# Optimization experiments

Hardware: AMD Instinct MI355X
Metric: run time of the kernel (lower is better)

The kernel has to match this reference:

```python
import jax, jax.numpy as jnp
import numpy as np

NUM_QUERIES, NUM_KEYS = 32, 64
QUERY_DIM, KEY_DIM = 512, 512
NUM_HEADS, ATTN_DIM = 8, 64
EMBED_DIM = NUM_HEADS * ATTN_DIM  # 512
OUT_DIM = 512
TEMPERATURE = float(np.sqrt(ATTN_DIM))


def setup_inputs() -> dict:
    key = jax.random.key(0)
    ks = jax.random.split(key, 6)
    b = 1.0 / TEMPERATURE
    b_p = 1.0 / float(np.sqrt(OUT_DIM))
    q = jax.random.normal(ks[0], (NUM_QUERIES, 2048, QUERY_DIM), dtype=jnp.float32)
    k = jax.random.normal(ks[1], (NUM_KEYS, 2048, KEY_DIM), dtype=jnp.float32)
    query_weight = jax.random.uniform(ks[2], (NUM_QUERIES, QUERY_DIM, EMBED_DIM), minval=-b, maxval=b, dtype=jnp.float32)
    key_weight = jax.random.uniform(ks[3], (NUM_KEYS, KEY_DIM, EMBED_DIM), minval=-b, maxval=b, dtype=jnp.float32)
    value_weight = jax.random.uniform(ks[4], (NUM_KEYS, KEY_DIM, EMBED_DIM), minval=-b, maxval=b, dtype=jnp.float32)
    proj_weight = jax.random.uniform(ks[5], (NUM_QUERIES, EMBED_DIM, OUT_DIM), minval=-b_p, maxval=b_p, dtype=jnp.float32)
    return {"q": q, "k": k, "query_weight": query_weight, "key_weight": key_weight,
            "value_weight": value_weight, "proj_weight": proj_weight}


def reference(q, k, query_weight, key_weight, value_weight, proj_weight):
    Qn, bs, _ = q.shape
    Kn = k.shape[0]
    H, D = NUM_HEADS, ATTN_DIM
    # per-slot projections: (slots, bs, embed) -> split embed into heads
    query = jnp.einsum('ibq,iqe->ibe', q, query_weight).reshape(Qn, bs, H, D)
    key_e = jnp.einsum('jbk,jke->jbe', k, key_weight).reshape(Kn, bs, H, D)
    value = jnp.einsum('jbk,jke->jbe', k, value_weight).reshape(Kn, bs, H, D)
    # logits over key slots per (batch, head, query slot)
    logits = jnp.einsum('ibhd,jbhd->bhij', query, key_e) / TEMPERATURE
    attn = jax.nn.softmax(logits, axis=-1)  # softmax over key slots
    out = jnp.einsum('bhij,jbhd->ibhd', attn, value).reshape(Qn, bs, H * D)
    out = jnp.einsum('ibe,ieo->ibo', out, proj_weight)
    return out
```

## Files before the change

### kernel.cpp

```cpp
#include <hip/hip_runtime.h>

typedef __attribute__((ext_vector_type(8))) short bf16x8;
typedef __attribute__((ext_vector_type(4))) float f32x4;
typedef __attribute__((ext_vector_type(4))) unsigned short us4;

__device__ __forceinline__ unsigned short f2bf(float f) {
    unsigned u = __builtin_bit_cast(unsigned, f);
    u += 0x7FFFu + ((u >> 16) & 1u);
    return (unsigned short)(u >> 16);
}

__device__ __forceinline__ void gl_lds16(const void* g, void* l) {
    __builtin_amdgcn_global_load_lds(
        (const __attribute__((address_space(1))) unsigned int*)g,
        (__attribute__((address_space(3))) unsigned int*)l, 16, 0, 0);
}

__global__ __launch_bounds__(256) void cast_f32_bf16(const float* __restrict__ in,
                                                     unsigned short* __restrict__ out, int n4) {
    int i = blockIdx.x * blockDim.x + threadIdx.x;
    int stride = gridDim.x * blockDim.x;
    for (; i < n4; i += stride) {
        float4 v = ((const float4*)in)[i];
        us4 o;
        o.x = f2bf(v.x); o.y = f2bf(v.y); o.z = f2bf(v.z); o.w = f2bf(v.w);
        ((us4*)out)[i] = o;
    }
}

__global__ __launch_bounds__(256) void transpose_w(const float* __restrict__ wq,
                                                   const float* __restrict__ wk,
                                                   const float* __restrict__ wv,
                                                   const float* __restrict__ wp,
                                                   unsigned short* __restrict__ Wt) {
    int sb = blockIdx.x >> 6;
    int tile = blockIdx.x & 63;
    const float* src;
    if (sb < 32)       src = wq + (size_t)sb * 262144;
    else if (sb < 96)  src = wk + (size_t)(sb - 32) * 262144;
    else if (sb < 160) src = wv + (size_t)(sb - 96) * 262144;
    else               src = wp + (size_t)(sb - 160) * 262144;
    unsigned short* dst = Wt + (size_t)sb * 262144;
    int q0 = (tile & 7) * 64, e0 = (tile >> 3) * 64;
    __shared__ float t[64][65];
    int tx = threadIdx.x & 63, ty = threadIdx.x >> 6;
    for (int i = 0; i < 16; i++) {
        int r = ty + 4 * i;
        t[r][tx] = src[(size_t)(q0 + r) * 512 + e0 + tx];
    }
    __syncthreads();
    int tx2 = threadIdx.x & 31, ty2 = threadIdx.x >> 5;
    for (int i = 0; i < 8; i++) {
        int e = ty2 + 8 * i;
        int qq = tx2 * 2;
        unsigned a = f2bf(t[qq][e]);
        unsigned bb = f2bf(t[qq + 1][e]);
        *(unsigned*)&dst[(size_t)(e0 + e) * 512 + q0 + qq] = a | (bb << 16);
    }
}

__device__ __forceinline__ void gemm256(const unsigned short* __restrict__ Ag,
                                        const unsigned short* __restrict__ Bg,
                                        unsigned short (&lds)[2][2][16384],
                                        f32x4 (&acc)[8][4]) {
    const int tid = threadIdx.x;
    const int l = tid & 63, wid = tid >> 6;
    const int wr = (wid >> 2) * 128, wc = (wid & 3) * 64;
    const int lr = l & 15, shi = l >> 4;
    const int srcs = ((l & 7) ^ ((l >> 3) & 7)) * 8;
    const int grow = l >> 3;

    bf16x8 af[4][2], bf[2][2][2];

#define STG_(which, hh, t) do {                                                     \
    const unsigned short* gp = (which) ? Bg : Ag;                                   \
    _Pragma("unroll")                                                               \
    for (int q = 0; q < 2; q++) {                                                   \
        int lrow = (hh) * 128 + wid * 16 + q * 8;                                   \
        gl_lds16(gp + (size_t)(lrow + grow) * 512 + (t) * 64 + srcs,                \
                 &lds[(t) & 1][which][lrow * 64]);                                  \
    } } while (0)

#define LDA_(cur, mh) do {                                                          \
    _Pragma("unroll") for (int m = 0; m < 4; m++)                                   \
    _Pragma("unroll") for (int ks = 0; ks < 2; ks++)                                \
        af[m][ks] = *(const bf16x8*)&lds[cur][0]                                    \
            [(wr + (mh) * 64 + m * 16 + lr) * 64 + ((ks * 4 + shi) ^ (l & 7)) * 8]; \
    } while (0)

#define LDB_(cur, nh) do {                                                          \
    _Pragma("unroll") for (int n = 0; n < 2; n++)                                   \
    _Pragma("unroll") for (int ks = 0; ks < 2; ks++)                                \
        bf[nh][n][ks] = *(const bf16x8*)&lds[cur][1]                                \
            [(wc + (nh) * 32 + n * 16 + lr) * 64 + ((ks * 4 + shi) ^ (l & 7)) * 8]; \
    } while (0)

#define MM_(mh, nh) do {                                                            \
    __builtin_amdgcn_s_setprio(1);                                                  \
    _Pragma("unroll") for (int m = 0; m < 4; m++)                                   \
    _Pragma("unroll") for (int n = 0; n < 2; n++)                                   \
    _Pragma("unroll") for (int ks = 0; ks < 2; ks++)                                \
        acc[(mh) * 4 + m][(nh) * 2 + n] = __builtin_amdgcn_mfma_f32_16x16x32_bf16(  \
            af[m][ks], bf[nh][n][ks], acc[(mh) * 4 + m][(nh) * 2 + n], 0, 0, 0);    \
    __builtin_amdgcn_s_setprio(0);                                                  \
    } while (0)

#define FENCE_ asm volatile("" ::: "memory")
#define BAR_ do { FENCE_; __builtin_amdgcn_s_barrier(); FENCE_; } while (0)

    STG_(0, 0, 0); STG_(0, 1, 0); STG_(1, 0, 0); STG_(1, 1, 0);
    STG_(1, 0, 1); STG_(1, 1, 1);
    asm volatile("s_waitcnt vmcnt(4)" ::: "memory");
    BAR_;

#pragma unroll
    for (int i = 0; i < 4; i++) {
        LDA_(0, 0); LDB_(0, 0);
        STG_(0, 0, 2 * i + 1);
        BAR_; MM_(0, 0); BAR_;
        LDB_(0, 1);
        STG_(0, 1, 2 * i + 1);
        BAR_; MM_(0, 1); BAR_;
        LDA_(0, 1);
        if (i < 3) STG_(1, 0, 2 * i + 2);
        BAR_; MM_(1, 0); BAR_;
        if (i < 3) STG_(1, 1, 2 * i + 2);
        BAR_; MM_(1, 1);
        if (i < 3) asm volatile("s_waitcnt vmcnt(4)" ::: "memory");
        else       asm volatile("s_waitcnt vmcnt(0)" ::: "memory");
        BAR_;
        LDA_(1, 0); LDB_(1, 0);
        if (i < 3) STG_(0, 0, 2 * i + 2);
        BAR_; MM_(0, 0); BAR_;
        LDB_(1, 1);
        if (i < 3) STG_(0, 1, 2 * i + 2);
        BAR_; MM_(0, 1); BAR_;
        LDA_(1, 1);
        if (i <= 2) STG_(1, 0, 2 * i + 3);
        BAR_; MM_(1, 0); BAR_;
        if (i <= 2) STG_(1, 1, 2 * i + 3);
        BAR_; MM_(1, 1);
        if (i < 3) asm volatile("s_waitcnt vmcnt(4)" ::: "memory");
        else       asm volatile("s_waitcnt vmcnt(0)" ::: "memory");
        BAR_;
    }
#undef STG_
#undef LDA_
#undef LDB_
#undef MM_
}

__global__ __launch_bounds__(512, 1) void gemm_qkv(const unsigned short* __restrict__ qb,
                                                   const unsigned short* __restrict__ kb,
                                                   const unsigned short* __restrict__ Wt,
                                                   unsigned short* __restrict__ Qs,
                                                   unsigned short* __restrict__ Ks,
                                                   unsigned short* __restrict__ Vs) {
    __shared__ __align__(16) unsigned short lds[2][2][16384];
    int bid = blockIdx.x;
    int logical = (bid & 7) * 320 + (bid >> 3);
    int sIdx, x;
    if (logical < 512) {
        int grp = logical >> 5, w = logical & 31;
        sIdx = grp * 2 + (w & 1);
        x = w >> 1;
    } else {
        int p = (logical - 512) >> 5, w = (logical - 512) & 31;
        sIdx = 32 + p * 2 + (w & 1);
        x = w >> 1;
    }
    int tm = x >> 1, tn = x & 1;
    const unsigned short* A;
    unsigned short* Cw;
    int wslot;
    if (sIdx < 32) {
        A = qb + (size_t)sIdx * 1048576; Cw = Qs + (size_t)sIdx * 1048576; wslot = sIdx;
    } else {
        int pp = sIdx - 32, ks = pp >> 1;
        A = kb + (size_t)ks * 1048576;
        if (pp & 1) { Cw = Vs + (size_t)ks * 1048576; wslot = 96 + ks; }
        else        { Cw = Ks + (size_t)ks * 1048576; wslot = 32 + ks; }
    }
    const unsigned short* B = Wt + (size_t)wslot * 262144;
    const unsigned short* Ag = A + (size_t)(tm * 256) * 512;
    const unsigned short* Bg = B + (size_t)(tn * 256) * 512;

    f32x4 acc[8][4] = {};
    gemm256(Ag, Bg, lds, acc);

    const int l = threadIdx.x & 63, wid = threadIdx.x >> 6;
    const int wm = wid >> 2, wc = (wid & 3) * 64;
    unsigned short* Cs = &lds[0][0][0];
    for (int pass = 0; pass < 2; pass++) {
        __syncthreads();
        if (wm == pass) {
            for (int m = 0; m < 8; m++)
                for (int n = 0; n < 4; n++)
                    for (int r = 0; r < 4; r++)
                        Cs[(m * 16 + (l >> 4) * 4 + r) * 264 + wc + n * 16 + (l & 15)] = f2bf(acc[m][n][r]);
        }
        __syncthreads();
        for (int rnd = 0; rnd < 8; rnd++) {
            int idx = rnd * 512 + threadIdx.x;
            int row = idx >> 5, c8 = (idx & 31) * 8;
            bf16x8 v = *(const bf16x8*)&Cs[row * 264 + c8];
            *(bf16x8*)&Cw[(size_t)(tm * 256 + pass * 128 + row) * 512 + tn * 256 + c8] = v;
        }
    }
}

__global__ __launch_bounds__(512, 1) void gemm_proj(const unsigned short* __restrict__ Ain,
                                                    const unsigned short* __restrict__ Wt,
                                                    float* __restrict__ out) {
    __shared__ __align__(16) unsigned short lds[2][2][16384];
    int bid = blockIdx.x;
    int logical = (bid & 7) * 64 + (bid >> 3);
    int s = logical >> 4, x = logical & 15;
    int tm = x >> 1, tn = x & 1;
    const unsigned short* A = Ain + (size_t)s * 1048576;
    const unsigned short* B = Wt + (size_t)(160 + s) * 262144;
    const unsigned short* Ag = A + (size_t)(tm * 256) * 512;
    const unsigned short* Bg = B + (size_t)(tn * 256) * 512;

    f32x4 acc[8][4] = {};
    gemm256(Ag, Bg, lds, acc);

    const int l = threadIdx.x & 63, wid = threadIdx.x >> 6;
    const int wm = wid >> 2, wc = (wid & 3) * 64;
    float* Cf = (float*)&lds[0][0][0];
    for (int pass = 0; pass < 4; pass++) {
        __syncthreads();
        if (wm == (pass >> 1)) {
            int mb = (pass & 1) * 4;
            for (int mm = 0; mm < 4; mm++)
                for (int n = 0; n < 4; n++)
                    for (int r = 0; r < 4; r++)
                        Cf[(mm * 16 + (l >> 4) * 4 + r) * 260 + wc + n * 16 + (l & 15)] = acc[mb + mm][n][r];
        }
        __syncthreads();
        for (int rnd = 0; rnd < 8; rnd++) {
            int idx = rnd * 512 + threadIdx.x;
            int row = idx >> 6, c4 = (idx & 63) * 4;
            float4 v = *(const float4*)&Cf[row * 260 + c4];
            *(float4*)&out[(size_t)s * 1048576 + (size_t)(tm * 256 + pass * 64 + row) * 512 + tn * 256 + c4] = v;
        }
    }
}

__global__ __launch_bounds__(256) void attn_k(const unsigned short* __restrict__ Qs,
                                              const unsigned short* __restrict__ Ks,
                                              const unsigned short* __restrict__ Vs,
                                              unsigned short* __restrict__ Aout) {
    __shared__ __align__(16) unsigned short pl[4][32 * 72];
    __shared__ __align__(16) unsigned short vt[4][64 * 88];
    const size_t SL = 1048576;
    int w = threadIdx.x >> 6, l = threadIdx.x & 63;
    int g = blockIdx.x * 4 + w;
    int b = g >> 3, h = g & 7;
    const unsigned short* Qp = Qs + (size_t)b * 512 + h * 64;
    const unsigned short* Kp = Ks + (size_t)b * 512 + h * 64;
    const unsigned short* Vp = Vs + (size_t)b * 512 + h * 64;
    int lr = l & 15, lc = l >> 4;
    unsigned short* vtw = vt[w];

    for (int jr = 0; jr < 64; jr += 8) {
        int j = jr + (l >> 3), d0 = (l & 7) * 8;
        bf16x8 v = *(const bf16x8*)&Vp[(size_t)j * SL + d0];
        for (int e = 0; e < 8; e++) vtw[(d0 + e) * 88 + j] = (unsigned short)v[e];
    }

    bf16x8 aQ[2][2], bK[4][2];
    for (int m = 0; m < 2; m++)
        for (int kc = 0; kc < 2; kc++)
            aQ[m][kc] = *(const bf16x8*)&Qp[(size_t)(m * 16 + lr) * SL + kc * 32 + lc * 8];
    for (int n = 0; n < 4; n++)
        for (int kc = 0; kc < 2; kc++)
            bK[n][kc] = *(const bf16x8*)&Kp[(size_t)(n * 16 + lr) * SL + kc * 32 + lc * 8];

    f32x4 acc[2][4] = {};
    for (int kc = 0; kc < 2; kc++)
        for (int m = 0; m < 2; m++)
            for (int n = 0; n < 4; n++)
                acc[m][n] = __builtin_amdgcn_mfma_f32_16x16x32_bf16(aQ[m][kc], bK[n][kc], acc[m][n], 0, 0, 0);

    const float sc = 0.18033688011112042f;
    for (int m = 0; m < 2; m++) {
        for (int r = 0; r < 4; r++) {
            float v = acc[m][0][r];
            for (int n = 1; n < 4; n++) v = fmaxf(v, acc[m][n][r]);
            for (int sh = 1; sh < 16; sh <<= 1) v = fmaxf(v, __shfl_xor(v, sh));
            float ssum = 0.f;
            for (int n = 0; n < 4; n++) {
                float p = exp2f((acc[m][n][r] - v) * sc);
                acc[m][n][r] = p;
                ssum += p;
            }
            for (int sh = 1; sh < 16; sh <<= 1) ssum += __shfl_xor(ssum, sh);
            float inv = 1.0f / ssum;
            for (int n = 0; n < 4; n++)
                pl[w][(m * 16 + lc * 4 + r) * 72 + n * 16 + lr] = f2bf(acc[m][n][r] * inv);
        }
    }

    bf16x8 aP[2][2], bV[4][2];
    for (int m = 0; m < 2; m++)
        for (int kc = 0; kc < 2; kc++)
            aP[m][kc] = *(const bf16x8*)&pl[w][(m * 16 + lr) * 72 + kc * 32 + lc * 8];
    for (int n = 0; n < 4; n++)
        for (int kc = 0; kc < 2; kc++)
            bV[n][kc] = *(const bf16x8*)&vtw[(n * 16 + lr) * 88 + kc * 32 + lc * 8];

    f32x4 o[2][4] = {};
    for (int kc = 0; kc < 2; kc++)
        for (int m = 0; m < 2; m++)
            for (int n = 0; n < 4; n++)
                o[m][n] = __builtin_amdgcn_mfma_f32_16x16x32_bf16(aP[m][kc], bV[n][kc], o[m][n], 0, 0, 0);

    for (int m = 0; m < 2; m++)
        for (int n = 0; n < 4; n++)
            for (int r = 0; r < 4; r++)
                vtw[(m * 16 + lc * 4 + r) * 88 + n * 16 + lr] = f2bf(o[m][n][r]);
    for (int rnd = 0; rnd < 4; rnd++) {
        int i = rnd * 8 + (l >> 3), d0 = (l & 7) * 8;
        bf16x8 v = *(const bf16x8*)&vtw[i * 88 + d0];
        *(bf16x8*)&Aout[(size_t)i * SL + (size_t)b * 512 + h * 64 + d0] = v;
    }
}

extern "C" void kernel_launch(void* const* d_in, const int* in_sizes, int n_in,
                              void* d_out, int out_size, void* d_ws, size_t ws_size,
                              hipStream_t stream) {
    const float* q  = (const float*)d_in[0];
    const float* k  = (const float*)d_in[1];
    const float* wq = (const float*)d_in[2];
    const float* wk = (const float*)d_in[3];
    const float* wv = (const float*)d_in[4];
    const float* wp = (const float*)d_in[5];

    char* ws = (char*)d_ws;
    unsigned short* qb = (unsigned short*)(ws);
    unsigned short* kb = (unsigned short*)(ws + ((size_t)64 << 20));
    unsigned short* Wt = (unsigned short*)(ws + ((size_t)192 << 20));
    unsigned short* Qs = (unsigned short*)(ws + ((size_t)288 << 20));
    unsigned short* Ks = (unsigned short*)(ws + ((size_t)352 << 20));
    unsigned short* Vs = (unsigned short*)(ws + ((size_t)480 << 20));
    unsigned short* Aout = qb;
    float* out = (float*)d_out;

    hipLaunchKernelGGL(cast_f32_bf16, dim3(2048), dim3(256), 0, stream, q, qb, 32 * 2048 * 512 / 4);
    hipLaunchKernelGGL(cast_f32_bf16, dim3(2048), dim3(256), 0, stream, k, kb, 64 * 2048 * 512 / 4);
    hipLaunchKernelGGL(transpose_w, dim3(192 * 64), dim3(256), 0, stream, wq, wk, wv, wp, Wt);
    hipLaunchKernelGGL(gemm_qkv, dim3(2560), dim3(512), 0, stream, qb, kb, Wt, Qs, Ks, Vs);
    hipLaunchKernelGGL(attn_k, dim3(4096), dim3(256), 0, stream, Qs, Ks, Vs, Aout);
    hipLaunchKernelGGL(gemm_proj, dim3(512), dim3(512), 0, stream, Aout, Wt, out);
}
```

Baseline: 552.4 us.

## Fuse fp32-to-bf16 input cast into QKV GEMM and use head-major QKV layout

Drops the separate cast kernels for q and k. The QKV GEMM now loads fp32 A tiles into registers, converts them with packed bf16 conversion, and writes them into swizzled LDS, interleaved with the existing double-buffered B staging. The QKV outputs are also written in a [batch][head][slot][dim] layout, so the attention kernel reads contiguous per-(batch, head) blocks instead of gathering with a 1M-element stride. The cost removed is a full read and write of the bf16 copies of q and k plus launch overhead. In exchange, the GEMM reads fp32 A, which is twice the bytes per tile, and each of the two tn tiles converts the same A rows, so the register-staged pipeline has more latency to hide.

```diff
diff --git a/kernel.cpp b/kernel.cpp
--- a/kernel.cpp
+++ b/kernel.cpp
@@ -14,18 +14,6 @@
     __builtin_amdgcn_global_load_lds(
         (const __attribute__((address_space(1))) unsigned int*)g,
         (__attribute__((address_space(3))) unsigned int*)l, 16, 0, 0);
-}
-
-__global__ __launch_bounds__(256) void cast_f32_bf16(const float* __restrict__ in,
-                                                     unsigned short* __restrict__ out, int n4) {
-    int i = blockIdx.x * blockDim.x + threadIdx.x;
-    int stride = gridDim.x * blockDim.x;
-    for (; i < n4; i += stride) {
-        float4 v = ((const float4*)in)[i];
-        us4 o;
-        o.x = f2bf(v.x); o.y = f2bf(v.y); o.z = f2bf(v.z); o.w = f2bf(v.w);
-        ((us4*)out)[i] = o;
-    }
 }
 
 __global__ __launch_bounds__(256) void transpose_w(const float* __restrict__ wq,
@@ -145,17 +133,113 @@
         BAR_;
     }
 #undef STG_
+}
+
+__device__ __forceinline__ void gemm256f(const float* __restrict__ Af,
+                                         const unsigned short* __restrict__ Bg,
+                                         unsigned short (&lds)[2][2][16384],
+                                         f32x4 (&acc)[8][4]) {
+    const int tid = threadIdx.x;
+    const int l = tid & 63, wid = tid >> 6;
+    const int wr = (wid >> 2) * 128, wc = (wid & 3) * 64;
+    const int lr = l & 15, shi = l >> 4;
+    const int srcs = ((l & 7) ^ ((l >> 3) & 7)) * 8;
+    const int grow = l >> 3;
+    const int arow = l >> 4;
+    const int acol = (l & 15) * 4;
+    const int aslot = (l & 15) >> 1;
+    const int ahalf = (l & 1) * 4;
+
+    float4 rA0[4], rA1[4];
+    bf16x8 af[4][2], bf[2][2][2];
+
+#define TC_(t) ((t) > 7 ? 7 : (t))
+
+#define LOADA_(R, hh, t) do {                                                       \
+    _Pragma("unroll")                                                               \
+    for (int q = 0; q < 4; q++)                                                     \
+        R[q] = *(const float4*)&Af[(size_t)((hh) * 128 + wid * 16 + q * 4 + arow)   \
+                                   * 512 + (t) * 64 + acol];                        \
+    } while (0)
+
+#define WRITEA_(R, hh, t) do {                                                      \
+    _Pragma("unroll")                                                               \
+    for (int q = 0; q < 4; q++) {                                                   \
+        int r_ = (hh) * 128 + wid * 16 + q * 4 + arow;                              \
+        unsigned lo_, hi_;                                                          \
+        asm("v_cvt_pk_bf16_f32 %0, %1, %2" : "=v"(lo_) : "v"(R[q].x), "v"(R[q].y)); \
+        asm("v_cvt_pk_bf16_f32 %0, %1, %2" : "=v"(hi_) : "v"(R[q].z), "v"(R[q].w)); \
+        uint2 pk_; pk_.x = lo_; pk_.y = hi_;                                        \
+        *(uint2*)&lds[(t) & 1][0][r_ * 64 + ((aslot ^ (r_ & 7)) << 3) + ahalf] = pk_; \
+    } } while (0)
+
+#define STGB_(hh, t) do {                                                           \
+    _Pragma("unroll")                                                               \
+    for (int q = 0; q < 2; q++) {                                                   \
+        int lrow = (hh) * 128 + wid * 16 + q * 8;                                   \
+        gl_lds16(Bg + (size_t)(lrow + grow) * 512 + (t) * 64 + srcs,                \
+                 &lds[(t) & 1][1][lrow * 64]);                                      \
+    } } while (0)
+
+#define LGKM0_ asm volatile("s_waitcnt lgkmcnt(0)" ::: "memory")
+#define VM12_  asm volatile("s_waitcnt vmcnt(12)" ::: "memory")
+
+    LOADA_(rA0, 0, 0); LOADA_(rA1, 1, 0);
+    STGB_(0, 0); STGB_(1, 0);
+    WRITEA_(rA0, 0, 0); WRITEA_(rA1, 1, 0);
+    LOADA_(rA0, 0, 1); LOADA_(rA1, 1, 1);
+    STGB_(0, 1); STGB_(1, 1);
+    LGKM0_;
+    VM12_;
+    BAR_;
+
+#pragma unroll
+    for (int i = 0; i < 4; i++) {
+        const int t1 = 2 * i + 1, t2 = TC_(2 * i + 2), t3 = TC_(2 * i + 3);
+        LDA_(0, 0); LDB_(0, 0);
+        WRITEA_(rA0, 0, t1);
+        LGKM0_; BAR_; MM_(0, 0); BAR_;
+        LDB_(0, 1);
+        WRITEA_(rA1, 1, t1);
+        LGKM0_; BAR_; MM_(0, 1); BAR_;
+        LDA_(0, 1);
+        LOADA_(rA0, 0, t2); STGB_(0, t2);
+        BAR_; MM_(1, 0); BAR_;
+        LOADA_(rA1, 1, t2); STGB_(1, t2);
+        BAR_; MM_(1, 1); VM12_; BAR_;
+        LDA_(1, 0); LDB_(1, 0);
+        WRITEA_(rA0, 0, t2);
+        LOADA_(rA0, 0, t3);
+        LGKM0_; BAR_; MM_(0, 0); BAR_;
+        LDB_(1, 1);
+        WRITEA_(rA1, 1, t2);
+        LOADA_(rA1, 1, t3);
+        LGKM0_; BAR_; MM_(0, 1); BAR_;
+        LDA_(1, 1);
+        STGB_(0, t3);
+        BAR_; MM_(1, 0); BAR_;
+        STGB_(1, t3);
+        BAR_; MM_(1, 1); VM12_; BAR_;
+    }
+    asm volatile("s_waitcnt vmcnt(0)" ::: "memory");
+    LGKM0_;
+#undef TC_
+#undef LOADA_
+#undef WRITEA_
+#undef STGB_
+#undef LGKM0_
+#undef VM12_
 #undef LDA_
 #undef LDB_
 #undef MM_
 }
 
-__global__ __launch_bounds__(512, 1) void gemm_qkv(const unsigned short* __restrict__ qb,
-                                                   const unsigned short* __restrict__ kb,
+__global__ __launch_bounds__(512, 1) void gemm_qkv(const float* __restrict__ qf,
+                                                   const float* __restrict__ kf,
                                                    const unsigned short* __restrict__ Wt,
-                                                   unsigned short* __restrict__ Qs,
-                                                   unsigned short* __restrict__ Ks,
-                                                   unsigned short* __restrict__ Vs) {
+                                                   unsigned short* __restrict__ Qg,
+                                                   unsigned short* __restrict__ Kg,
+                                                   unsigned short* __restrict__ Vg) {
     __shared__ __align__(16) unsigned short lds[2][2][16384];
     int bid = blockIdx.x;
     int logical = (bid & 7) * 320 + (bid >> 3);
@@ -170,23 +254,25 @@
         x = w >> 1;
     }
     int tm = x >> 1, tn = x & 1;
-    const unsigned short* A;
+    const float* Afull;
     unsigned short* Cw;
-    int wslot;
+    int wslot, slot, nslots;
     if (sIdx < 32) {
-        A = qb + (size_t)sIdx * 1048576; Cw = Qs + (size_t)sIdx * 1048576; wslot = sIdx;
+        Afull = qf + (size_t)sIdx * 1048576;
+        Cw = Qg; wslot = sIdx; slot = sIdx; nslots = 32;
     } else {
         int pp = sIdx - 32, ks = pp >> 1;
-        A = kb + (size_t)ks * 1048576;
-        if (pp & 1) { Cw = Vs + (size_t)ks * 1048576; wslot = 96 + ks; }
-        else        { Cw = Ks + (size_t)ks * 1048576; wslot = 32 + ks; }
+        Afull = kf + (size_t)ks * 1048576;
+        if (pp & 1) { Cw = Vg; wslot = 96 + ks; }
+        else        { Cw = Kg; wslot = 32 + ks; }
+        slot = ks; nslots = 64;
     }
     const unsigned short* B = Wt + (size_t)wslot * 262144;
-    const unsigned short* Ag = A + (size_t)(tm * 256) * 512;
+    const float* Ag = Afull + (size_t)(tm * 256) * 512;
     const unsigned short* Bg = B + (size_t)(tn * 256) * 512;
 
     f32x4 acc[8][4] = {};
-    gemm256(Ag, Bg, lds, acc);
+    gemm256f(Ag, Bg, lds, acc);
 
     const int l = threadIdx.x & 63, wid = threadIdx.x >> 6;
     const int wm = wid >> 2, wc = (wid & 3) * 64;
@@ -204,7 +290,10 @@
             int idx = rnd * 512 + threadIdx.x;
             int row = idx >> 5, c8 = (idx & 31) * 8;
             bf16x8 v = *(const bf16x8*)&Cs[row * 264 + c8];
-            *(bf16x8*)&Cw[(size_t)(tm * 256 + pass * 128 + row) * 512 + tn * 256 + c8] = v;
+            int bb = tm * 256 + pass * 128 + row;
+            int e0 = tn * 256 + c8;
+            int h = e0 >> 6, d0 = e0 & 63;
+            *(bf16x8*)&Cw[(((size_t)bb * 8 + h) * nslots + slot) * 64 + d0] = v;
         }
     }
 }
@@ -247,9 +336,9 @@
     }
 }
 
-__global__ __launch_bounds__(256) void attn_k(const unsigned short* __restrict__ Qs,
-                                              const unsigned short* __restrict__ Ks,
-                                              const unsigned short* __restrict__ Vs,
+__global__ __launch_bounds__(256) void attn_k(const unsigned short* __restrict__ Qg,
+                                              const unsigned short* __restrict__ Kg,
+                                              const unsigned short* __restrict__ Vg,
                                               unsigned short* __restrict__ Aout) {
     __shared__ __align__(16) unsigned short pl[4][32 * 72];
     __shared__ __align__(16) unsigned short vt[4][64 * 88];
@@ -257,25 +346,25 @@
     int w = threadIdx.x >> 6, l = threadIdx.x & 63;
     int g = blockIdx.x * 4 + w;
     int b = g >> 3, h = g & 7;
-    const unsigned short* Qp = Qs + (size_t)b * 512 + h * 64;
-    const unsigned short* Kp = Ks + (size_t)b * 512 + h * 64;
-    const unsigned short* Vp = Vs + (size_t)b * 512 + h * 64;
+    const unsigned short* Qp = Qg + (size_t)(b * 8 + h) * 2048;
+    const unsigned short* Kp = Kg + (size_t)(b * 8 + h) * 4096;
+    const unsigned short* Vp = Vg + (size_t)(b * 8 + h) * 4096;
     int lr = l & 15, lc = l >> 4;
     unsigned short* vtw = vt[w];
 
     for (int jr = 0; jr < 64; jr += 8) {
         int j = jr + (l >> 3), d0 = (l & 7) * 8;
-        bf16x8 v = *(const bf16x8*)&Vp[(size_t)j * SL + d0];
+        bf16x8 v = *(const bf16x8*)&Vp[j * 64 + d0];
         for (int e = 0; e < 8; e++) vtw[(d0 + e) * 88 + j] = (unsigned short)v[e];
     }
 
     bf16x8 aQ[2][2], bK[4][2];
     for (int m = 0; m < 2; m++)
         for (int kc = 0; kc < 2; kc++)
-            aQ[m][kc] = *(const bf16x8*)&Qp[(size_t)(m * 16 + lr) * SL + kc * 32 + lc * 8];
+            aQ[m][kc] = *(const bf16x8*)&Qp[(m * 16 + lr) * 64 + kc * 32 + lc * 8];
     for (int n = 0; n < 4; n++)
         for (int kc = 0; kc < 2; kc++)
-            bK[n][kc] = *(const bf16x8*)&Kp[(size_t)(n * 16 + lr) * SL + kc * 32 + lc * 8];
+            bK[n][kc] = *(const bf16x8*)&Kp[(n * 16 + lr) * 64 + kc * 32 + lc * 8];
 
     f32x4 acc[2][4] = {};
     for (int kc = 0; kc < 2; kc++)
@@ -338,19 +427,15 @@
     const float* wp = (const float*)d_in[5];
 
     char* ws = (char*)d_ws;
-    unsigned short* qb = (unsigned short*)(ws);
-    unsigned short* kb = (unsigned short*)(ws + ((size_t)64 << 20));
+    unsigned short* Aout = (unsigned short*)(ws);
     unsigned short* Wt = (unsigned short*)(ws + ((size_t)192 << 20));
-    unsigned short* Qs = (unsigned short*)(ws + ((size_t)288 << 20));
-    unsigned short* Ks = (unsigned short*)(ws + ((size_t)352 << 20));
-    unsigned short* Vs = (unsigned short*)(ws + ((size_t)480 << 20));
-    unsigned short* Aout = qb;
+    unsigned short* Qg = (unsigned short*)(ws + ((size_t)288 << 20));
+    unsigned short* Kg = (unsigned short*)(ws + ((size_t)352 << 20));
+    unsigned short* Vg = (unsigned short*)(ws + ((size_t)480 << 20));
     float* out = (float*)d_out;
 
-    hipLaunchKernelGGL(cast_f32_bf16, dim3(2048), dim3(256), 0, stream, q, qb, 32 * 2048 * 512 / 4);
-    hipLaunchKernelGGL(cast_f32_bf16, dim3(2048), dim3(256), 0, stream, k, kb, 64 * 2048 * 512 / 4);
     hipLaunchKernelGGL(transpose_w, dim3(192 * 64), dim3(256), 0, stream, wq, wk, wv, wp, Wt);
-    hipLaunchKernelGGL(gemm_qkv, dim3(2560), dim3(512), 0, stream, qb, kb, Wt, Qs, Ks, Vs);
-    hipLaunchKernelGGL(attn_k, dim3(4096), dim3(256), 0, stream, Qs, Ks, Vs, Aout);
+    hipLaunchKernelGGL(gemm_qkv, dim3(2560), dim3(512), 0, stream, q, k, Wt, Qg, Kg, Vg);
+    hipLaunchKernelGGL(attn_k, dim3(4096), dim3(256), 0, stream, Qg, Kg, Vg, Aout);
     hipLaunchKernelGGL(gemm_proj, dim3(512), dim3(512), 0, stream, Aout, Wt, out);
 }
```

New measurement: 1.052 ms. 1.9x slower.

## Simplify GEMM main loop to one LDS tile per iteration with fewer barriers

Applied to the files above, without the earlier changes.

Replaces the hand-unrolled 4x2 half-tile schedule in gemm256 with a uniform 8-iteration loop. Each iteration loads the full B fragment once and runs two MFMA batches over the A halves. Global-to-LDS staging for the next A tile and the tile-after-next B are issued at fixed points. This halves the number of workgroup barriers per K tile and simplifies the prefetch pattern. In exchange, the overlap between staging and MFMA shifts and each MFMA batch waits on larger fragment loads.

```diff
diff --git a/kernel.cpp b/kernel.cpp
--- a/kernel.cpp
+++ b/kernel.cpp
@@ -15,6 +15,9 @@
         (const __attribute__((address_space(1))) unsigned int*)g,
         (__attribute__((address_space(3))) unsigned int*)l, 16, 0, 0);
 }
+
+#define FENCE_ asm volatile("" ::: "memory")
+#define BAR_ do { FENCE_; __builtin_amdgcn_s_barrier(); FENCE_; } while (0)
 
 __global__ __launch_bounds__(256) void cast_f32_bf16(const float* __restrict__ in,
                                                      unsigned short* __restrict__ out, int n4) {
@@ -70,7 +73,7 @@
     const int srcs = ((l & 7) ^ ((l >> 3) & 7)) * 8;
     const int grow = l >> 3;
 
-    bf16x8 af[4][2], bf[2][2][2];
+    bf16x8 af[4][2], bf[4][2];
 
 #define STG_(which, hh, t) do {                                                     \
     const unsigned short* gp = (which) ? Bg : Ag;                                   \
@@ -88,61 +91,41 @@
             [(wr + (mh) * 64 + m * 16 + lr) * 64 + ((ks * 4 + shi) ^ (l & 7)) * 8]; \
     } while (0)
 
-#define LDB_(cur, nh) do {                                                          \
-    _Pragma("unroll") for (int n = 0; n < 2; n++)                                   \
+#define LDB_(cur) do {                                                             \
+    _Pragma("unroll") for (int n = 0; n < 4; n++)                                   \
     _Pragma("unroll") for (int ks = 0; ks < 2; ks++)                                \
-        bf[nh][n][ks] = *(const bf16x8*)&lds[cur][1]                                \
-            [(wc + (nh) * 32 + n * 16 + lr) * 64 + ((ks * 4 + shi) ^ (l & 7)) * 8]; \
+        bf[n][ks] = *(const bf16x8*)&lds[cur][1]                                    \
+            [(wc + n * 16 + lr) * 64 + ((ks * 4 + shi) ^ (l & 7)) * 8];             \
     } while (0)
 
-#define MM_(mh, nh) do {                                                            \
+#define MM_(mh) do {                                                                \
     __builtin_amdgcn_s_setprio(1);                                                  \
     _Pragma("unroll") for (int m = 0; m < 4; m++)                                   \
-    _Pragma("unroll") for (int n = 0; n < 2; n++)                                   \
+    _Pragma("unroll") for (int n = 0; n < 4; n++)                                   \
     _Pragma("unroll") for (int ks = 0; ks < 2; ks++)                                \
-        acc[(mh) * 4 + m][(nh) * 2 + n] = __builtin_amdgcn_mfma_f32_16x16x32_bf16(  \
-            af[m][ks], bf[nh][n][ks], acc[(mh) * 4 + m][(nh) * 2 + n], 0, 0, 0);    \
+        acc[(mh) * 4 + m][n] = __builtin_amdgcn_mfma_f32_16x16x32_bf16(             \
+            af[m][ks], bf[n][ks], acc[(mh) * 4 + m][n], 0, 0, 0);                   \
     __builtin_amdgcn_s_setprio(0);                                                  \
     } while (0)
 
-#define FENCE_ asm volatile("" ::: "memory")
-#define BAR_ do { FENCE_; __builtin_amdgcn_s_barrier(); FENCE_; } while (0)
-
-    STG_(0, 0, 0); STG_(0, 1, 0); STG_(1, 0, 0); STG_(1, 1, 0);
+    STG_(0, 0, 0); STG_(0, 1, 0);
+    STG_(1, 0, 0); STG_(1, 1, 0);
     STG_(1, 0, 1); STG_(1, 1, 1);
     asm volatile("s_waitcnt vmcnt(4)" ::: "memory");
     BAR_;
 
 #pragma unroll
-    for (int i = 0; i < 4; i++) {
-        LDA_(0, 0); LDB_(0, 0);
-        STG_(0, 0, 2 * i + 1);
-        BAR_; MM_(0, 0); BAR_;
-        LDB_(0, 1);
-        STG_(0, 1, 2 * i + 1);
-        BAR_; MM_(0, 1); BAR_;
-        LDA_(0, 1);
-        if (i < 3) STG_(1, 0, 2 * i + 2);
-        BAR_; MM_(1, 0); BAR_;
-        if (i < 3) STG_(1, 1, 2 * i + 2);
-        BAR_; MM_(1, 1);
-        if (i < 3) asm volatile("s_waitcnt vmcnt(4)" ::: "memory");
-        else       asm volatile("s_waitcnt vmcnt(0)" ::: "memory");
-        BAR_;
-        LDA_(1, 0); LDB_(1, 0);
-        if (i < 3) STG_(0, 0, 2 * i + 2);
-        BAR_; MM_(0, 0); BAR_;
-        LDB_(1, 1);
-        if (i < 3) STG_(0, 1, 2 * i + 2);
-        BAR_; MM_(0, 1); BAR_;
-        LDA_(1, 1);
-        if (i <= 2) STG_(1, 0, 2 * i + 3);
-        BAR_; MM_(1, 0); BAR_;
-        if (i <= 2) STG_(1, 1, 2 * i + 3);
-        BAR_; MM_(1, 1);
-        if (i < 3) asm volatile("s_waitcnt vmcnt(4)" ::: "memory");
-        else       asm volatile("s_waitcnt vmcnt(0)" ::: "memory");
-        BAR_;
+    for (int t = 0; t < 8; t++) {
+        const int cur = t & 1;
+        if (t < 7) { STG_(0, 0, t + 1); STG_(0, 1, t + 1); }
+        LDA_(cur, 0); LDB_(cur);
+        BAR_; MM_(0); BAR_;
+        if (t < 6) { STG_(1, 0, t + 2); STG_(1, 1, t + 2); }
+        LDA_(cur, 1);
+        BAR_; MM_(1);
+        if (t < 6)       asm volatile("s_waitcnt vmcnt(4)" ::: "memory");
+        else if (t == 6) asm volatile("s_waitcnt vmcnt(0)" ::: "memory");
+        if (t < 7) BAR_;
     }
 #undef STG_
 #undef LDA_
```

New measurement: 554.4 us. No clear change (+0.4%).
